# Optimization experiments

Hardware: AMD Instinct MI355X
Metric: run time of the kernel (lower is better)

The kernel has to match this reference:

```python
import jax, jax.numpy as jnp
import numpy as np
from jax import lax

K = 12          # filterbank order (units per group)
G = 2           # number of groups / filterbanks
T_SAMP = 1.0    # samp_interval
B, S = 2048, 2048


def setup_inputs() -> dict:
    key = jax.random.key(0)
    k1, k2 = jax.random.split(key)
    x = jax.random.normal(k1, (B, S, G), dtype=jnp.float32)
    # relax in (0.2, 0.8) so sqrt(relax) and sqrt(1-relax) are well-behaved
    relax = 0.2 + 0.6 * jax.random.uniform(k2, (G,), dtype=jnp.float32)
    return {"x": x, "relax": relax}


def reference(x, relax):
    """Laguerre FilterbankCell unrolled over time with lax.scan.

    x:     [B, S, G] input sequence (one channel per filterbank group)
    relax: [G]       per-group relaxation parameter in (0,1)
    returns [B, S, G, K] filterbank outputs per timestep.
    """
    sa = jnp.sqrt(relax)            # sqrt(relax_i),    [G]
    sb = jnp.sqrt(1.0 - relax)      # sqrt(1-relax_i),  [G]

    def step(prev, xt):
        # prev: [B, G, K] previous filterbank state; xt: [B, G]
        y0 = sa[None, :] * prev[:, :, 0] + T_SAMP * sb[None, :] * xt  # [B, G]
        ys = [y0]
        for j in range(1, K):  # K is small and fixed -> unrolled lag chain
            yj = sa[None, :] * prev[:, :, j] + sa[None, :] * ys[-1] - prev[:, :, j - 1]
            ys.append(yj)
        y = jnp.stack(ys, axis=2)  # [B, G, K]
        return y, y

    init = jnp.zeros((x.shape[0], G, K), dtype=x.dtype)
    xs = jnp.moveaxis(x, 1, 0)                 # [S, B, G]
    _, outs = lax.scan(step, init, xs)         # [S, B, G, K]
    return jnp.moveaxis(outs, 0, 1)            # [B, S, G, K]
```

## Files before the change

kernel.cpp:

```cpp
#include <hip/hip_runtime.h>


#define KF 12
#define GF 2
#define BF 2048
#define SF 2048
#define BG (BF * GF)

__device__ __forceinline__ void fb_step2(float* __restrict__ y0, float* __restrict__ y1,
                                         float x0, float x1,
                                         float sa0, float tsb0, float sa1, float tsb1) {
    float pm0 = y0[0], pm1 = y1[0];
    y0[0] = fmaf(sa0, y0[0], tsb0 * x0);
    y1[0] = fmaf(sa1, y1[0], tsb1 * x1);
    #pragma unroll
    for (int j = 1; j < KF; ++j) {
        const float t0 = y0[j], t1 = y1[j];
        y0[j] = fmaf(sa0, t0, fmaf(sa0, y0[j - 1], -pm0));
        y1[j] = fmaf(sa1, t1, fmaf(sa1, y1[j - 1], -pm1));
        pm0 = t0; pm1 = t1;
    }
}

template <int NC>
__global__ void setup_mpow(const float* __restrict__ relax, float* __restrict__ Mp) {
    constexpr int LCH = SF / NC;
    constexpr int LOG2L = (LCH == 16) ? 4 : ((LCH == 32) ? 5 : 6);
    const int g = blockIdx.x;
    const int t = threadIdx.x;
    __shared__ float A[KF][KF];
    const float rx = relax[g];
    const float sa = sqrtf(rx);

    if (t < KF * KF) {
        const int j = t / KF, m = t % KF;
        float v = 0.0f;
        if (m == j) {
            v = sa;
        } else if (m < j) {
            float p = 1.0f;
            for (int i = 0; i < j - m - 1; ++i) p *= sa;
            v = -(1.0f - rx) * p;
        }
        A[j][m] = v;
    }
    __syncthreads();

    for (int it = 0; it < LOG2L; ++it) {
        float s = 0.0f;
        if (t < KF * KF) {
            const int j = t / KF, m = t % KF;
            #pragma unroll
            for (int i = 0; i < KF; ++i) s += A[j][i] * A[i][m];
        }
        __syncthreads();
        if (t < KF * KF) A[t / KF][t % KF] = s;
        __syncthreads();
    }

    if (t < KF * KF) Mp[g * KF * KF + t] = A[t / KF][t % KF];
}

template <int NC>
__global__ __launch_bounds__(256, 4) void pass1_chunk_states(
        const float* __restrict__ x, const float* __restrict__ relax,
        float* __restrict__ F) {
    constexpr int LCH = SF / NC;
    const int tid = blockIdx.x * 256 + threadIdx.x;
    const int c = tid & (NC - 1);
    const int b = tid / NC;

    const float r0 = relax[0], r1 = relax[1];
    const float sa0 = sqrtf(r0), tsb0 = sqrtf(1.0f - r0);
    const float sa1 = sqrtf(r1), tsb1 = sqrtf(1.0f - r1);

    float y0[KF], y1[KF];
    #pragma unroll
    for (int k = 0; k < KF; ++k) { y0[k] = 0.0f; y1[k] = 0.0f; }

    const float4* xp = (const float4*)(x + ((size_t)b * SF + (size_t)c * LCH) * GF);
    for (int t2 = 0; t2 < LCH / 2; ++t2) {
        const float4 xv = xp[t2];
        fb_step2(y0, y1, xv.x, xv.y, sa0, tsb0, sa1, tsb1);
        fb_step2(y0, y1, xv.z, xv.w, sa0, tsb0, sa1, tsb1);
    }

    float4* Fp = (float4*)(F + ((size_t)b * NC + c) * (GF * KF));
    Fp[0] = make_float4(y0[0], y0[1], y0[2],  y0[3]);
    Fp[1] = make_float4(y0[4], y0[5], y0[6],  y0[7]);
    Fp[2] = make_float4(y0[8], y0[9], y0[10], y0[11]);
    Fp[3] = make_float4(y1[0], y1[1], y1[2],  y1[3]);
    Fp[4] = make_float4(y1[4], y1[5], y1[6],  y1[7]);
    Fp[5] = make_float4(y1[8], y1[9], y1[10], y1[11]);
}

template <int NC>
__global__ void pass2_combine(float* __restrict__ F, const float* __restrict__ Mp) {
    const int tid = blockIdx.x * blockDim.x + threadIdx.x;
    const int sub = tid & 15;
    const int bg  = tid >> 4;
    const int b   = bg >> 1;
    const int g   = bg & 1;
    const int lane = threadIdx.x & 63;
    const int grpbase = lane & ~15;

    const int k = (sub < KF) ? sub : 0;
    float Mrow[KF];
    const float* mr = Mp + ((size_t)g * KF + k) * KF;
    #pragma unroll
    for (int m = 0; m < KF; ++m) Mrow[m] = mr[m];

    float* Fb = F + ((size_t)b * NC) * (GF * KF) + g * KF + k;

    float r = 0.0f;
    float fnext = Fb[0];
    for (int c = 1; c < NC; ++c) {
        const float fcur = fnext;
        if (c + 1 < NC) fnext = Fb[(size_t)c * (GF * KF)];
        float acc = fcur;
        #pragma unroll
        for (int m = 0; m < KF; ++m) {
            acc += Mrow[m] * __shfl(r, grpbase + m, 64);
        }
        if (sub < KF) Fb[(size_t)(c - 1) * (GF * KF)] = acc;
        r = acc;
    }
}

__device__ __forceinline__ void stage24(char* Lw, int kbase, int sswz,
                                        const float* __restrict__ y0,
                                        const float* __restrict__ y1) {
    *(float4*)(Lw + ((kbase +  0) ^ sswz)) = make_float4(y0[0], y0[1], y0[2],  y0[3]);
    *(float4*)(Lw + ((kbase + 16) ^ sswz)) = make_float4(y0[4], y0[5], y0[6],  y0[7]);
    *(float4*)(Lw + ((kbase + 32) ^ sswz)) = make_float4(y0[8], y0[9], y0[10], y0[11]);
    *(float4*)(Lw + ((kbase + 48) ^ sswz)) = make_float4(y1[0], y1[1], y1[2],  y1[3]);
    *(float4*)(Lw + ((kbase + 64) ^ sswz)) = make_float4(y1[4], y1[5], y1[6],  y1[7]);
    *(float4*)(Lw + ((kbase + 80) ^ sswz)) = make_float4(y1[8], y1[9], y1[10], y1[11]);
}

template <int NC>
__global__ __launch_bounds__(128) void pass3_outputs(
        const float* __restrict__ x, const float* __restrict__ relax,
        const float* __restrict__ F, float* __restrict__ out) {
    constexpr int LCH   = SF / NC;
    constexpr int WPB   = NC / 64;
    constexpr int NWIN  = LCH / 4;
    constexpr int ROWF4 = LCH * 6;
    __shared__ __align__(16) float lds[2 * 64 * 96];

    const int lane = threadIdx.x & 63;
    const int w    = threadIdx.x >> 6;
    const int W    = blockIdx.x * 2 + w;
    const int b    = W / WPB;
    const int c0   = (W % WPB) * 64;
    const int c    = c0 + lane;

    const float r0 = relax[0], r1 = relax[1];
    const float sa0 = sqrtf(r0), tsb0 = sqrtf(1.0f - r0);
    const float sa1 = sqrtf(r1), tsb1 = sqrtf(1.0f - r1);

    float y0[KF], y1[KF];
    if (c == 0) {
        #pragma unroll
        for (int k = 0; k < KF; ++k) { y0[k] = 0.0f; y1[k] = 0.0f; }
    } else {
        const float4* Fp = (const float4*)(F + ((size_t)b * NC + (c - 1)) * (GF * KF));
        const float4 a0 = Fp[0], a1 = Fp[1], a2 = Fp[2];
        const float4 a3 = Fp[3], a4 = Fp[4], a5 = Fp[5];
        y0[0] = a0.x; y0[1] = a0.y; y0[2]  = a0.z; y0[3]  = a0.w;
        y0[4] = a1.x; y0[5] = a1.y; y0[6]  = a1.z; y0[7]  = a1.w;
        y0[8] = a2.x; y0[9] = a2.y; y0[10] = a2.z; y0[11] = a2.w;
        y1[0] = a3.x; y1[1] = a3.y; y1[2]  = a3.z; y1[3]  = a3.w;
        y1[4] = a4.x; y1[5] = a4.y; y1[6]  = a4.z; y1[7]  = a4.w;
        y1[8] = a5.x; y1[9] = a5.y; y1[10] = a5.z; y1[11] = a5.w;
    }

    char* Lw = (char*)&lds[w * 64 * 96];
    const int sbase = lane * 384;
    const int sswz  = (lane & 7) << 4;

    int gof[24], lof[24];
    #pragma unroll
    for (int j = 0; j < 24; ++j) {
        const int v  = j * 64 + lane;
        const int cf = v / 24;
        const int qf = v - cf * 24;
        gof[j] = (c0 + cf) * ROWF4 + qf;
        lof[j] = (cf * 384 + qf * 16) ^ ((cf & 7) << 4);
    }

    const float4* xp = (const float4*)(x + ((size_t)b * SF + (size_t)c * LCH) * GF);
    float4* outb = (float4*)(out + (size_t)b * SF * (GF * KF));

    for (int win = 0; win < NWIN; ++win) {
        const float4 xa = xp[2 * win];
        const float4 xb = xp[2 * win + 1];

        fb_step2(y0, y1, xa.x, xa.y, sa0, tsb0, sa1, tsb1);
        stage24(Lw, sbase +   0, sswz, y0, y1);
        fb_step2(y0, y1, xa.z, xa.w, sa0, tsb0, sa1, tsb1);
        stage24(Lw, sbase +  96, sswz, y0, y1);
        fb_step2(y0, y1, xb.x, xb.y, sa0, tsb0, sa1, tsb1);
        stage24(Lw, sbase + 192, sswz, y0, y1);
        fb_step2(y0, y1, xb.z, xb.w, sa0, tsb0, sa1, tsb1);
        stage24(Lw, sbase + 288, sswz, y0, y1);

        const int tof = win * 24;
        #pragma unroll
        for (int j = 0; j < 24; ++j) {
            outb[(size_t)(gof[j] + tof)] = *(const float4*)(Lw + lof[j]);
        }
    }
}

template <int NC>
static void run_all(const float* x, const float* relax, float* out,
                    float* Mp, float* F, hipStream_t stream) {
    setup_mpow<NC><<<GF, 192, 0, stream>>>(relax, Mp);
    pass1_chunk_states<NC><<<(BF * NC) / 256, 256, 0, stream>>>(x, relax, F);
    pass2_combine<NC><<<(BG * 16) / 256, 256, 0, stream>>>(F, Mp);
    pass3_outputs<NC><<<(BF * (NC / 64)) / 2, 128, 0, stream>>>(x, relax, F, out);
}

extern "C" void kernel_launch(void* const* d_in, const int* in_sizes, int n_in,
                              void* d_out, int out_size, void* d_ws, size_t ws_size,
                              hipStream_t stream) {
    const float* x     = (const float*)d_in[0];
    const float* relax = (const float*)d_in[1];
    float* out = (float*)d_out;

    float* Mp = (float*)d_ws;
    float* F  = (float*)((char*)d_ws + 4096);

    const size_t need128 = 4096 + (size_t)BF * 128 * (GF * KF) * sizeof(float);
    if (ws_size >= need128) {
        run_all<128>(x, relax, out, Mp, F, stream);
    } else {
        run_all<64>(x, relax, out, Mp, F, stream);
    }
}
```

Before: 488.2 us.

## Fold matrix-power setup into combine pass and use nontemporal output stores

Removes the separate matrix-power setup kernel by computing the chunk-transfer matrix power redundantly in shared memory inside every combine block, saving one launch. Deepens the prefetch of chunk states in the combine loop, shrinks the output pass to one wavefront per block, unrolls its window loop by two, and writes outputs with nontemporal stores to reduce cache pollution on the large output write. The trade-off is redundant matrix work in every combine block and a changed occupancy for the output pass.

```diff
diff --git a/kernel.cpp b/kernel.cpp
--- a/kernel.cpp
+++ b/kernel.cpp
@@ -6,6 +6,8 @@
 #define BF 2048
 #define SF 2048
 #define BG (BF * GF)
+
+typedef float f32x4 __attribute__((ext_vector_type(4)));
 
 __device__ __forceinline__ void fb_step2(float* __restrict__ y0, float* __restrict__ y1,
                                          float x0, float x1,
@@ -23,17 +25,52 @@
 }
 
 template <int NC>
-__global__ void setup_mpow(const float* __restrict__ relax, float* __restrict__ Mp) {
+__global__ __launch_bounds__(256, 4) void pass1_chunk_states(
+        const float* __restrict__ x, const float* __restrict__ relax,
+        float* __restrict__ F) {
+    constexpr int LCH = SF / NC;
+    const int tid = blockIdx.x * 256 + threadIdx.x;
+    const int c = tid & (NC - 1);
+    const int b = tid / NC;
+
+    const float r0 = relax[0], r1 = relax[1];
+    const float sa0 = sqrtf(r0), tsb0 = sqrtf(1.0f - r0);
+    const float sa1 = sqrtf(r1), tsb1 = sqrtf(1.0f - r1);
+
+    float y0[KF], y1[KF];
+    #pragma unroll
+    for (int k = 0; k < KF; ++k) { y0[k] = 0.0f; y1[k] = 0.0f; }
+
+    const float4* xp = (const float4*)(x + ((size_t)b * SF + (size_t)c * LCH) * GF);
+    for (int t2 = 0; t2 < LCH / 2; ++t2) {
+        const float4 xv = xp[t2];
+        fb_step2(y0, y1, xv.x, xv.y, sa0, tsb0, sa1, tsb1);
+        fb_step2(y0, y1, xv.z, xv.w, sa0, tsb0, sa1, tsb1);
+    }
+
+    float4* Fp = (float4*)(F + ((size_t)b * NC + c) * (GF * KF));
+    Fp[0] = make_float4(y0[0], y0[1], y0[2],  y0[3]);
+    Fp[1] = make_float4(y0[4], y0[5], y0[6],  y0[7]);
+    Fp[2] = make_float4(y0[8], y0[9], y0[10], y0[11]);
+    Fp[3] = make_float4(y1[0], y1[1], y1[2],  y1[3]);
+    Fp[4] = make_float4(y1[4], y1[5], y1[6],  y1[7]);
+    Fp[5] = make_float4(y1[8], y1[9], y1[10], y1[11]);
+}
+
+template <int NC>
+__global__ __launch_bounds__(256) void pass2_combine(
+        float* __restrict__ F, const float* __restrict__ relax) {
     constexpr int LCH = SF / NC;
     constexpr int LOG2L = (LCH == 16) ? 4 : ((LCH == 32) ? 5 : 6);
-    const int g = blockIdx.x;
-    const int t = threadIdx.x;
-    __shared__ float A[KF][KF];
-    const float rx = relax[g];
-    const float sa = sqrtf(rx);
-
-    if (t < KF * KF) {
+    __shared__ float A[GF][KF][KF];
+    __shared__ float Btmp[GF][KF][KF];
+
+    for (int e = threadIdx.x; e < GF * KF * KF; e += 256) {
+        const int g = e / (KF * KF);
+        const int t = e % (KF * KF);
         const int j = t / KF, m = t % KF;
+        const float rx = relax[g];
+        const float sa = sqrtf(rx);
         float v = 0.0f;
         if (m == j) {
             v = sa;
@@ -42,61 +79,30 @@
             for (int i = 0; i < j - m - 1; ++i) p *= sa;
             v = -(1.0f - rx) * p;
         }
-        A[j][m] = v;
+        A[g][j][m] = v;
     }
     __syncthreads();
 
     for (int it = 0; it < LOG2L; ++it) {
-        float s = 0.0f;
-        if (t < KF * KF) {
+        for (int e = threadIdx.x; e < GF * KF * KF; e += 256) {
+            const int g = e / (KF * KF);
+            const int t = e % (KF * KF);
             const int j = t / KF, m = t % KF;
+            float s = 0.0f;
             #pragma unroll
-            for (int i = 0; i < KF; ++i) s += A[j][i] * A[i][m];
+            for (int i = 0; i < KF; ++i) s += A[g][j][i] * A[g][i][m];
+            Btmp[g][j][m] = s;
         }
         __syncthreads();
-        if (t < KF * KF) A[t / KF][t % KF] = s;
+        for (int e = threadIdx.x; e < GF * KF * KF; e += 256) {
+            const int g = e / (KF * KF);
+            const int t = e % (KF * KF);
+            A[g][t / KF][t % KF] = Btmp[g][t / KF][t % KF];
+        }
         __syncthreads();
     }
 
-    if (t < KF * KF) Mp[g * KF * KF + t] = A[t / KF][t % KF];
-}
-
-template <int NC>
-__global__ __launch_bounds__(256, 4) void pass1_chunk_states(
-        const float* __restrict__ x, const float* __restrict__ relax,
-        float* __restrict__ F) {
-    constexpr int LCH = SF / NC;
     const int tid = blockIdx.x * 256 + threadIdx.x;
-    const int c = tid & (NC - 1);
-    const int b = tid / NC;
-
-    const float r0 = relax[0], r1 = relax[1];
-    const float sa0 = sqrtf(r0), tsb0 = sqrtf(1.0f - r0);
-    const float sa1 = sqrtf(r1), tsb1 = sqrtf(1.0f - r1);
-
-    float y0[KF], y1[KF];
-    #pragma unroll
-    for (int k = 0; k < KF; ++k) { y0[k] = 0.0f; y1[k] = 0.0f; }
-
-    const float4* xp = (const float4*)(x + ((size_t)b * SF + (size_t)c * LCH) * GF);
-    for (int t2 = 0; t2 < LCH / 2; ++t2) {
-        const float4 xv = xp[t2];
-        fb_step2(y0, y1, xv.x, xv.y, sa0, tsb0, sa1, tsb1);
-        fb_step2(y0, y1, xv.z, xv.w, sa0, tsb0, sa1, tsb1);
-    }
-
-    float4* Fp = (float4*)(F + ((size_t)b * NC + c) * (GF * KF));
-    Fp[0] = make_float4(y0[0], y0[1], y0[2],  y0[3]);
-    Fp[1] = make_float4(y0[4], y0[5], y0[6],  y0[7]);
-    Fp[2] = make_float4(y0[8], y0[9], y0[10], y0[11]);
-    Fp[3] = make_float4(y1[0], y1[1], y1[2],  y1[3]);
-    Fp[4] = make_float4(y1[4], y1[5], y1[6],  y1[7]);
-    Fp[5] = make_float4(y1[8], y1[9], y1[10], y1[11]);
-}
-
-template <int NC>
-__global__ void pass2_combine(float* __restrict__ F, const float* __restrict__ Mp) {
-    const int tid = blockIdx.x * blockDim.x + threadIdx.x;
     const int sub = tid & 15;
     const int bg  = tid >> 4;
     const int b   = bg >> 1;
@@ -106,18 +112,19 @@
 
     const int k = (sub < KF) ? sub : 0;
     float Mrow[KF];
-    const float* mr = Mp + ((size_t)g * KF + k) * KF;
-    #pragma unroll
-    for (int m = 0; m < KF; ++m) Mrow[m] = mr[m];
+    #pragma unroll
+    for (int m = 0; m < KF; ++m) Mrow[m] = A[g][k][m];
 
     float* Fb = F + ((size_t)b * NC) * (GF * KF) + g * KF + k;
 
     float r = 0.0f;
-    float fnext = Fb[0];
+    float f0 = Fb[0];
+    float f1 = Fb[GF * KF];
+    float f2 = Fb[2 * (GF * KF)];
     for (int c = 1; c < NC; ++c) {
-        const float fcur = fnext;
-        if (c + 1 < NC) fnext = Fb[(size_t)c * (GF * KF)];
-        float acc = fcur;
+        float acc = f0;
+        f0 = f1; f1 = f2;
+        if (c + 4 <= NC) f2 = Fb[(size_t)(c + 2) * (GF * KF)];
         #pragma unroll
         for (int m = 0; m < KF; ++m) {
             acc += Mrow[m] * __shfl(r, grpbase + m, 64);
@@ -139,18 +146,17 @@
 }
 
 template <int NC>
-__global__ __launch_bounds__(128) void pass3_outputs(
+__global__ __launch_bounds__(64) void pass3_outputs(
         const float* __restrict__ x, const float* __restrict__ relax,
         const float* __restrict__ F, float* __restrict__ out) {
     constexpr int LCH   = SF / NC;
     constexpr int WPB   = NC / 64;
     constexpr int NWIN  = LCH / 4;
     constexpr int ROWF4 = LCH * 6;
-    __shared__ __align__(16) float lds[2 * 64 * 96];
-
-    const int lane = threadIdx.x & 63;
-    const int w    = threadIdx.x >> 6;
-    const int W    = blockIdx.x * 2 + w;
+    __shared__ __align__(16) float lds[64 * 96];
+
+    const int lane = threadIdx.x;
+    const int W    = blockIdx.x;
     const int b    = W / WPB;
     const int c0   = (W % WPB) * 64;
     const int c    = c0 + lane;
@@ -175,7 +181,7 @@
         y1[8] = a5.x; y1[9] = a5.y; y1[10] = a5.z; y1[11] = a5.w;
     }
 
-    char* Lw = (char*)&lds[w * 64 * 96];
+    char* Lw = (char*)lds;
     const int sbase = lane * 384;
     const int sswz  = (lane & 7) << 4;
 
@@ -190,8 +196,9 @@
     }
 
     const float4* xp = (const float4*)(x + ((size_t)b * SF + (size_t)c * LCH) * GF);
-    float4* outb = (float4*)(out + (size_t)b * SF * (GF * KF));
-
+    f32x4* outb = (f32x4*)(out + (size_t)b * SF * (GF * KF));
+
+    #pragma unroll 2
     for (int win = 0; win < NWIN; ++win) {
         const float4 xa = xp[2 * win];
         const float4 xb = xp[2 * win + 1];
@@ -208,18 +215,18 @@
         const int tof = win * 24;
         #pragma unroll
         for (int j = 0; j < 24; ++j) {
-            outb[(size_t)(gof[j] + tof)] = *(const float4*)(Lw + lof[j]);
+            const f32x4 v = *(const f32x4*)(Lw + lof[j]);
+            __builtin_nontemporal_store(v, &outb[(size_t)(gof[j] + tof)]);
         }
     }
 }
 
 template <int NC>
 static void run_all(const float* x, const float* relax, float* out,
-                    float* Mp, float* F, hipStream_t stream) {
-    setup_mpow<NC><<<GF, 192, 0, stream>>>(relax, Mp);
+                    float* F, hipStream_t stream) {
     pass1_chunk_states<NC><<<(BF * NC) / 256, 256, 0, stream>>>(x, relax, F);
-    pass2_combine<NC><<<(BG * 16) / 256, 256, 0, stream>>>(F, Mp);
-    pass3_outputs<NC><<<(BF * (NC / 64)) / 2, 128, 0, stream>>>(x, relax, F, out);
+    pass2_combine<NC><<<(BG * 16) / 256, 256, 0, stream>>>(F, relax);
+    pass3_outputs<NC><<<BF * (NC / 64), 64, 0, stream>>>(x, relax, F, out);
 }
 
 extern "C" void kernel_launch(void* const* d_in, const int* in_sizes, int n_in,
@@ -229,13 +236,12 @@
     const float* relax = (const float*)d_in[1];
     float* out = (float*)d_out;
 
-    float* Mp = (float*)d_ws;
-    float* F  = (float*)((char*)d_ws + 4096);
-
-    const size_t need128 = 4096 + (size_t)BF * 128 * (GF * KF) * sizeof(float);
+    float* F = (float*)d_ws;
+
+    const size_t need128 = (size_t)BF * 128 * (GF * KF) * sizeof(float);
     if (ws_size >= need128) {
-        run_all<128>(x, relax, out, Mp, F, stream);
+        run_all<128>(x, relax, out, F, stream);
     } else {
-        run_all<64>(x, relax, out, Mp, F, stream);
-    }
-}
+        run_all<64>(x, relax, out, F, stream);
+    }
+}
```

Result: no change. 479.4 us (-1.8%).
